# Kernel tuning notes

Hardware: AMD Instinct MI355X
Metric: run time of the kernel (lower is better)

Reference implementation:

```python
import jax, jax.numpy as jnp
import numpy as np
import math

N = 8192       # number of cells (spatial tokens)
D = 512        # d_model
H = 512        # attn_hidden_dim (defaults to d_model)
GAMMA = 0.5    # real/fake mixing weight


def setup_inputs() -> dict:
    key = jax.random.key(0)
    ks = jax.random.split(key, 9)
    s = 1.0 / math.sqrt(D)  # nn.Linear-like init scale -> stable exp(scores)
    x = jax.random.normal(ks[0], (N, D), dtype=jnp.float32)
    real_edge_mask = jax.random.bernoulli(ks[1], 0.5, (N, N))
    fake_edge_mask = jax.random.bernoulli(ks[2], 0.5, (N, N))
    Wq_real = jax.random.normal(ks[3], (D, H), dtype=jnp.float32) * s
    Wk_real = jax.random.normal(ks[4], (D, H), dtype=jnp.float32) * s
    Wq_fake = jax.random.normal(ks[5], (D, H), dtype=jnp.float32) * s
    Wk_fake = jax.random.normal(ks[6], (D, H), dtype=jnp.float32) * s
    Wv = jax.random.normal(ks[7], (D, D), dtype=jnp.float32) * s
    bv = jnp.zeros((D,), dtype=jnp.float32)
    return dict(x=x, real_edge_mask=real_edge_mask, fake_edge_mask=fake_edge_mask,
                Wq_real=Wq_real, Wk_real=Wk_real, Wq_fake=Wq_fake, Wk_fake=Wk_fake,
                Wv=Wv, bv=bv)


def reference(x, real_edge_mask, fake_edge_mask, Wq_real, Wk_real, Wq_fake, Wk_fake, Wv, bv):
    scale = 1.0 / math.sqrt(H)
    neg = jnp.float32(-1e9)
    # real branch scores [N, N]
    sr = jnp.einsum('nh,mh->nm', x @ Wq_real, x @ Wk_real) * scale
    sr = jnp.where(real_edge_mask, neg, sr)
    # fake branch scores [N, N]
    sf = jnp.einsum('nh,mh->nm', x @ Wq_fake, x @ Wk_fake) * scale
    sf = jnp.where(fake_edge_mask, neg, sf)
    # NOTE: original computes row maxima but never uses them (dead code);
    # it exponentiates raw scores directly -- replicated faithfully.
    scores = (jnp.exp(sr) + GAMMA * jnp.exp(sf)) / (1.0 + GAMMA)
    attn = scores / jnp.sum(scores, axis=-1, keepdims=True)
    V = x @ Wv + bv
    cntx = attn @ V
    return cntx, attn
```

## Files before the change

kernel.cpp:

```cpp
#include <hip/hip_runtime.h>


#define K_N 8192
#define K_D 512

typedef float  f32x4 __attribute__((ext_vector_type(4)));
typedef _Float16 f16x8 __attribute__((ext_vector_type(8)));
typedef unsigned short u16;
typedef unsigned int u32;

__device__ __forceinline__ u16 f2h(float f) {
  _Float16 h = (_Float16)f;
  return __builtin_bit_cast(u16, h);
}
__device__ __forceinline__ float h2f(u16 b) {
  return (float)__builtin_bit_cast(_Float16, b);
}

__device__ __forceinline__ void gload_lds16(const void* g, void* l) {
  __builtin_amdgcn_global_load_lds(
      (const __attribute__((address_space(1))) void*)g,
      (__attribute__((address_space(3))) void*)l, 16, 0, 0);
}

__device__ __forceinline__ void nt_store4(float* p, f32x4 v) {
  __builtin_nontemporal_store(v, (f32x4*)p);
}

__global__ void k_detect(const unsigned char* __restrict__ m, int* __restrict__ flag) {
  __shared__ int any;
  if (threadIdx.x == 0) any = 0;
  __syncthreads();
  int local = 0;
  for (int i = threadIdx.x; i < 65536; i += 256)
    local |= m[4 * i + 1];
  if (local) atomicOr(&any, 1);
  __syncthreads();
  if (threadIdx.x == 0) *flag = any ? 1 : 0;
}

__device__ __forceinline__ bool mask_at(const void* mask, int mode, size_t idx) {
  if (mode) return ((const unsigned char*)mask)[idx] != 0;
  return ((const int*)mask)[idx] != 0;
}

__device__ __forceinline__ u32 pack_word(const void* m, int mode, int r, int c) {
  u32 out = 0;
  if (mode) {
    const uint4* p = (const uint4*)((const unsigned char*)m + (size_t)r * K_N + c * 32);
    uint4 a = p[0], b = p[1];
    u32 ws[8] = {a.x, a.y, a.z, a.w, b.x, b.y, b.z, b.w};
#pragma unroll
    for (int i = 0; i < 8; i++) {
      u32 v = ws[i];
      v |= v >> 4; v |= v >> 2; v |= v >> 1;
      v &= 0x01010101u;
      out |= (v & 1u) << (4 * i);
      out |= ((v >> 8) & 1u) << (4 * i + 1);
      out |= ((v >> 16) & 1u) << (4 * i + 2);
      out |= ((v >> 24) & 1u) << (4 * i + 3);
    }
  } else {
    const uint4* p = (const uint4*)((const int*)m + (size_t)r * K_N + c * 32);
#pragma unroll
    for (int i = 0; i < 8; i++) {
      uint4 v = p[i];
      out |= (v.x ? 1u : 0u) << (4 * i);
      out |= (v.y ? 1u : 0u) << (4 * i + 1);
      out |= (v.z ? 1u : 0u) << (4 * i + 2);
      out |= (v.w ? 1u : 0u) << (4 * i + 3);
    }
  }
  return out;
}

__global__ __launch_bounds__(256) void k_packmask2(
    const void* __restrict__ mR, const void* __restrict__ mF,
    const int* __restrict__ flag,
    u32* __restrict__ bR, u32* __restrict__ bF,
    float* __restrict__ cntx) {
  __shared__ u32 sm[32][129];
  const int mode = *flag;
  const int tid = threadIdx.x;
  const int r0 = blockIdx.x * 128;
  const int c0 = blockIdx.y * 32;

  {
    float4* cz = (float4*)cntx;
    int bid = blockIdx.x + (blockIdx.y << 6);
#pragma unroll
    for (int i = 0; i < 8; ++i)
      cz[(size_t)bid * 2048 + i * 256 + tid] = make_float4(0.f, 0.f, 0.f, 0.f);
  }

#pragma unroll
  for (int t = 0; t < 2; ++t) {
    const void* m = t ? mF : mR;
    u32* dst = t ? bF : bR;
    if (t) __syncthreads();
#pragma unroll 4
    for (int i = 0; i < 16; ++i) {
      int idx = i * 256 + tid;
      int r = idx >> 5, c = idx & 31;
      sm[c][r] = pack_word(m, mode, r0 + r, c0 + c);
    }
    __syncthreads();
#pragma unroll 4
    for (int i = 0; i < 16; ++i) {
      int idx = i * 256 + tid;
      int c = idx >> 7, r = idx & 127;
      dst[(size_t)(c0 + c) * K_N + r0 + r] = sm[c][r];
    }
  }
}

__global__ void k_transpose_w(const float* __restrict__ w0, const float* __restrict__ w1,
                              const float* __restrict__ w2, const float* __restrict__ w3,
                              const float* __restrict__ w4, u16* __restrict__ out) {
  __shared__ u16 sm[64][65];
  const float* srcs[5] = {w0, w1, w2, w3, w4};
  const float* in = srcs[blockIdx.z];
  u16* dst = out + (size_t)blockIdx.z * 262144;
  int c0 = blockIdx.x * 64, r0 = blockIdx.y * 64;
#pragma unroll
  for (int e = 0; e < 16; e++) {
    int idx = e * 256 + threadIdx.x;
    int i = idx >> 6, j = idx & 63;
    sm[i][j] = f2h(in[(size_t)(r0 + i) * 512 + c0 + j]);
  }
  __syncthreads();
#pragma unroll
  for (int e = 0; e < 16; e++) {
    int idx = e * 256 + threadIdx.x;
    int j = idx >> 6, i = idx & 63;
    dst[(size_t)(c0 + j) * 512 + r0 + i] = sm[i][j];
  }
}

__global__ void k_transpose_v(const u16* __restrict__ in, u16* __restrict__ out,
                              int R, int C) {
  __shared__ u16 sm[64][65];
  int c0 = blockIdx.x * 64, r0 = blockIdx.y * 64;
#pragma unroll
  for (int e = 0; e < 16; e++) {
    int idx = e * 256 + threadIdx.x;
    int i = idx >> 6, j = idx & 63;
    sm[i][j] = in[(size_t)(r0 + i) * C + c0 + j];
  }
  __syncthreads();
#pragma unroll
  for (int e = 0; e < 16; e++) {
    int idx = e * 256 + threadIdx.x;
    int j = idx >> 6, i = idx & 63;
    out[(size_t)(c0 + j) * R + r0 + i] = sm[i][j];
  }
}

template <int A_F32>
__device__ __forceinline__ void gemm_core(const void* __restrict__ Ap, int lda,
                                          const u16* __restrict__ Bt, int ldb,
                                          int rowBase, int colBase, int K,
                                          u16* sA, u16* sB, f32x4 (&acc)[4][4]) {
  const int tid   = threadIdx.x;
  const int lane  = tid & 63;
  const int waveM = tid >> 7;
  const int waveN = (tid >> 6) & 1;
  const int lrow  = lane & 15;
  const int lk    = lane >> 4;

  for (int k0 = 0; k0 < K; k0 += 64) {
    __syncthreads();
#pragma unroll
    for (int g = 0; g < 4; g++) {
      int cid = g * 256 + tid;
      int row = cid >> 3;
      int pk  = cid & 7;
      int k16 = pk ^ (row & 7);
      if (A_F32) {
        const float* s = (const float*)Ap + (size_t)(rowBase + row) * lda + k0 + k16 * 8;
        float4 v0 = *(const float4*)s;
        float4 v1 = *(const float4*)(s + 4);
        ushort4 h0, h1;
        h0.x = f2h(v0.x); h0.y = f2h(v0.y); h0.z = f2h(v0.z); h0.w = f2h(v0.w);
        h1.x = f2h(v1.x); h1.y = f2h(v1.y); h1.z = f2h(v1.z); h1.w = f2h(v1.w);
        *(ushort4*)&sA[cid * 8]     = h0;
        *(ushort4*)&sA[cid * 8 + 4] = h1;
      } else {
        uint4 v = *(const uint4*)((const u16*)Ap + (size_t)(rowBase + row) * lda + k0 + k16 * 8);
        *(uint4*)&sA[cid * 8] = v;
      }
      uint4 w = *(const uint4*)(Bt + (size_t)(colBase + row) * ldb + k0 + k16 * 8);
      *(uint4*)&sB[cid * 8] = w;
    }
    __syncthreads();
#pragma unroll
    for (int kk = 0; kk < 2; kk++) {
      f16x8 af[4], bfv[4];
      int k16 = kk * 4 + lk;
#pragma unroll
      for (int mb = 0; mb < 4; mb++) {
        int r = waveM * 64 + mb * 16 + lrow;
        af[mb] = *(const f16x8*)&sA[r * 64 + ((k16 ^ (r & 7)) << 3)];
      }
#pragma unroll
      for (int nb = 0; nb < 4; nb++) {
        int c = waveN * 64 + nb * 16 + lrow;
        bfv[nb] = *(const f16x8*)&sB[c * 64 + ((k16 ^ (c & 7)) << 3)];
      }
#pragma unroll
      for (int mb = 0; mb < 4; mb++)
#pragma unroll
        for (int nb = 0; nb < 4; nb++)
          acc[mb][nb] = __builtin_amdgcn_mfma_f32_16x16x32_f16(af[mb], bfv[nb], acc[mb][nb], 0, 0, 0);
    }
  }
}

__global__ __launch_bounds__(256) void k_proj(const float* __restrict__ x,
                                              const u16* __restrict__ wt,
                                              u16* __restrict__ qr, u16* __restrict__ kr,
                                              u16* __restrict__ qf, u16* __restrict__ kf,
                                              u16* __restrict__ vh,
                                              const float* __restrict__ bv) {
  __shared__ u16 sA[128 * 64], sB[128 * 64];
  f32x4 acc[4][4] = {};
  const int z = blockIdx.z;
  const int rowBase = blockIdx.y * 128, colBase = blockIdx.x * 128;
  gemm_core<1>(x, K_D, wt + (size_t)z * 262144, K_D, rowBase, colBase, K_D, sA, sB, acc);

  u16* out = (z == 0) ? qr : (z == 1) ? kr : (z == 2) ? qf : (z == 3) ? kf : vh;
  const int lane = threadIdx.x & 63;
  const int waveM = threadIdx.x >> 7, waveN = (threadIdx.x >> 6) & 1;
  const int lrow = lane & 15, lk = lane >> 4;
#pragma unroll
  for (int mb = 0; mb < 4; mb++)
#pragma unroll
    for (int nb = 0; nb < 4; nb++)
#pragma unroll
      for (int r = 0; r < 4; r++) {
        int grow = rowBase + waveM * 64 + mb * 16 + lk * 4 + r;
        int gcol = colBase + waveN * 64 + nb * 16 + lrow;
        float v = acc[mb][nb][r];
        if (z == 4) v += bv[gcol];
        out[(size_t)grow * K_D + gcol] = f2h(v);
      }
}

__global__ __launch_bounds__(256, 2) void k_scores2(
    const u16* __restrict__ qr, const u16* __restrict__ kr,
    const u16* __restrict__ qf, const u16* __restrict__ kf,
    const u32* __restrict__ bitR, const u32* __restrict__ bitF,
    u16* __restrict__ outp, float* __restrict__ partial) {

  __shared__ u16 s[2][2][8192];

  const int tid = threadIdx.x;
  const int lane = tid & 63, wid = tid >> 6;

  int b = blockIdx.x + (blockIdx.y << 6);
  int xcd = b & 7, j = b >> 3;
  const int by = xcd * 8 + (j & 7);
  const int bx = j >> 3;
  const int rowBase = by * 128, colBase = bx * 128;

  const u16* qrB = qr + (size_t)rowBase * K_D;
  const u16* krB = kr + (size_t)colBase * K_D;
  const u16* qfB = qf + (size_t)rowBase * K_D;
  const u16* kfB = kf + (size_t)colBase * K_D;

  f32x4 accR[4][4] = {}, accF[4][4] = {};

  auto STAGE = [&](int buf, const u16* qb, const u16* kb, int k0) {
#pragma unroll
    for (int jj = 0; jj < 4; ++jj) {
      int cid = jj * 256 + tid;
      int row = cid >> 3;
      int k16 = (cid & 7) ^ (row & 7);
      gload_lds16(qb + (size_t)row * K_D + k0 + k16 * 8,
                  &s[buf][0][(jj * 256 + wid * 64) * 8]);
      gload_lds16(kb + (size_t)row * K_D + k0 + k16 * 8,
                  &s[buf][1][(jj * 256 + wid * 64) * 8]);
    }
  };

  const int waveM = wid >> 1;
  const int waveN = wid & 1;
  const int lrow = lane & 15, lk = lane >> 4;

  auto COMPUTE = [&](f32x4 (&acc)[4][4], int cur) {
#pragma unroll
    for (int kk = 0; kk < 2; ++kk) {
      int k16 = kk * 4 + lk;
      f16x8 a[4], bb[4];
#pragma unroll
      for (int mb = 0; mb < 4; ++mb) {
        int r = waveM * 64 + mb * 16 + lrow;
        a[mb] = *(const f16x8*)&s[cur][0][r * 64 + ((k16 ^ (r & 7)) << 3)];
      }
#pragma unroll
      for (int nb = 0; nb < 4; ++nb) {
        int c = waveN * 64 + nb * 16 + lrow;
        bb[nb] = *(const f16x8*)&s[cur][1][c * 64 + ((k16 ^ (c & 7)) << 3)];
      }
#pragma unroll
      for (int mb = 0; mb < 4; ++mb)
#pragma unroll
        for (int nb = 0; nb < 4; ++nb)
          acc[mb][nb] = __builtin_amdgcn_mfma_f32_16x16x32_f16(a[mb], bb[nb], acc[mb][nb], 0, 0, 0);
    }
  };

  STAGE(0, qrB, krB, 0);
  __syncthreads();
  int cur = 0;
  for (int it = 0; it < 8; ++it) {
    if (it < 7) STAGE(cur ^ 1, qrB, krB, (it + 1) * 64);
    else        STAGE(cur ^ 1, qfB, kfB, 0);
    COMPUTE(accR, cur);
    __syncthreads();
    cur ^= 1;
  }
  for (int it = 0; it < 8; ++it) {
    if (it < 7) STAGE(cur ^ 1, qfB, kfB, (it + 1) * 64);
    COMPUTE(accF, cur);
    __syncthreads();
    cur ^= 1;
  }

  const float scale = 0.04419417382415922f;
  u16* vt16 = (u16*)&s[0][0][0];

#pragma unroll
  for (int mb = 0; mb < 4; ++mb)
#pragma unroll
    for (int rr = 0; rr < 4; ++rr) {
      int growl = waveM * 64 + mb * 16 + lk * 4 + rr;
      int grow = rowBase + growl;
      u32 wR0 = bitR[(size_t)(bx * 4 + waveN * 2 + 0) * K_N + grow];
      u32 wR1 = bitR[(size_t)(bx * 4 + waveN * 2 + 1) * K_N + grow];
      u32 wF0 = bitF[(size_t)(bx * 4 + waveN * 2 + 0) * K_N + grow];
      u32 wF1 = bitF[(size_t)(bx * 4 + waveN * 2 + 1) * K_N + grow];
      float rs = 0.f;
#pragma unroll
      for (int nb = 0; nb < 4; ++nb) {
        int cc = nb * 16 + lrow;
        int gcoll = waveN * 64 + cc;
        u32 wR = (cc >> 5) ? wR1 : wR0;
        u32 wF = (cc >> 5) ? wF1 : wF0;
        int bitpos = cc & 31;
        bool m1 = (wR >> bitpos) & 1u;
        bool m2 = (wF >> bitpos) & 1u;
        float er = m1 ? 0.f : __expf(accR[mb][nb][rr] * scale);
        float ef = m2 ? 0.f : __expf(accF[mb][nb][rr] * scale);
        float v = er + 0.5f * ef;
        rs += v;
        vt16[growl * 136 + gcoll] = f2h(v);
      }
      rs += __shfl_xor(rs, 1, 64);
      rs += __shfl_xor(rs, 2, 64);
      rs += __shfl_xor(rs, 4, 64);
      rs += __shfl_xor(rs, 8, 64);
      if (lrow == 0)
        partial[(size_t)grow * 128 + bx * 2 + waveN] = rs;
    }
  __syncthreads();

#pragma unroll
  for (int jj = 0; jj < 8; ++jj) {
    int f = jj * 256 + tid;
    int row = f >> 4, seg = f & 15;
    uint4 v = *(const uint4*)&vt16[row * 136 + seg * 8];
    *(uint4*)&outp[(size_t)(rowBase + row) * K_N + colBase + seg * 8] = v;
  }
}

template <int F16OUT, int USEBITS>
__global__ __launch_bounds__(512, 2) void k_scores8(
    const u16* __restrict__ qr, const u16* __restrict__ kr,
    const u16* __restrict__ qf, const u16* __restrict__ kf,
    const u32* __restrict__ bitR, const u32* __restrict__ bitF,
    const void* __restrict__ mR, const void* __restrict__ mF,
    const int* __restrict__ flag,
    void* __restrict__ outp, float* __restrict__ partial) {

  __shared__ u16 s[2][4][8192];

  const int tid = threadIdx.x;
  const int lane = tid & 63, wid = tid >> 6;
  const int bx = blockIdx.x, by = blockIdx.y;
  const int rowBase = by * 128, colBase = bx * 128;

  const u16* base0 = qr + (size_t)rowBase * K_D;
  const u16* base1 = kr + (size_t)colBase * K_D;
  const u16* base2 = qf + (size_t)rowBase * K_D;
  const u16* base3 = kf + (size_t)colBase * K_D;

  f32x4 accR[4][2] = {}, accF[4][2] = {};

  auto STAGE = [&](int b, int k0) {
    const u16* bases[4] = {base0, base1, base2, base3};
#pragma unroll
    for (int t = 0; t < 4; ++t)
#pragma unroll
      for (int j = 0; j < 2; ++j) {
        int cid = j * 512 + tid;
        int row = cid >> 3;
        int k16 = (cid & 7) ^ (row & 7);
        gload_lds16(bases[t] + (size_t)row * K_D + k0 + k16 * 8,
                    &s[b][t][(j * 512 + wid * 64) * 8]);
      }
  };

  STAGE(0, 0);
  __syncthreads();

  const int waveM = wid >> 2, waveN = wid & 3;
  const int lrow = lane & 15, lk = lane >> 4;

  int cur = 0;
  for (int it = 0; it < 8; ++it) {
    if (it < 7) STAGE(cur ^ 1, (it + 1) * 64);
#pragma unroll
    for (int kk = 0; kk < 2; ++kk) {
      int k16 = kk * 4 + lk;
      f16x8 aR[4], aF[4], bR[2], bF[2];
#pragma unroll
      for (int mb = 0; mb < 4; ++mb) {
        int r = waveM * 64 + mb * 16 + lrow;
        int off = r * 64 + ((k16 ^ (r & 7)) << 3);
        aR[mb] = *(const f16x8*)&s[cur][0][off];
        aF[mb] = *(const f16x8*)&s[cur][2][off];
      }
#pragma unroll
      for (int nb = 0; nb < 2; ++nb) {
        int c = waveN * 32 + nb * 16 + lrow;
        int off = c * 64 + ((k16 ^ (c & 7)) << 3);
        bR[nb] = *(const f16x8*)&s[cur][1][off];
        bF[nb] = *(const f16x8*)&s[cur][3][off];
      }
#pragma unroll
      for (int mb = 0; mb < 4; ++mb)
#pragma unroll
        for (int nb = 0; nb < 2; ++nb) {
          accR[mb][nb] = __builtin_amdgcn_mfma_f32_16x16x32_f16(aR[mb], bR[nb], accR[mb][nb], 0, 0, 0);
          accF[mb][nb] = __builtin_amdgcn_mfma_f32_16x16x32_f16(aF[mb], bF[nb], accF[mb][nb], 0, 0, 0);
        }
    }
    __syncthreads();
    cur ^= 1;
  }

  const float scale = 0.04419417382415922f;
  const int mode = USEBITS ? 0 : *flag;
  u16*   vt16 = (u16*)&s[0][0][0];
  float* vt32 = (float*)&s[0][0][0];

#pragma unroll
  for (int mb = 0; mb < 4; ++mb)
#pragma unroll
    for (int rr = 0; rr < 4; ++rr) {
      int growl = waveM * 64 + mb * 16 + lk * 4 + rr;
      int grow = rowBase + growl;
      u32 wR = 0, wF = 0;
      if (USEBITS) {
        wR = bitR[(size_t)(bx * 4 + waveN) * K_N + grow];
        wF = bitF[(size_t)(bx * 4 + waveN) * K_N + grow];
      }
      float rs = 0.f;
#pragma unroll
      for (int nb = 0; nb < 2; ++nb) {
        int bitpos = nb * 16 + lrow;
        int gcoll = waveN * 32 + bitpos;
        bool m1, m2;
        if (USEBITS) {
          m1 = (wR >> bitpos) & 1u;
          m2 = (wF >> bitpos) & 1u;
        } else {
          size_t oi = (size_t)grow * K_N + colBase + gcoll;
          m1 = mask_at(mR, mode, oi);
          m2 = mask_at(mF, mode, oi);
        }
        float er = m1 ? 0.f : __expf(accR[mb][nb][rr] * scale);
        float ef = m2 ? 0.f : __expf(accF[mb][nb][rr] * scale);
        float v = er + 0.5f * ef;
        rs += v;
        if (F16OUT) vt16[growl * 136 + gcoll] = f2h(v);
        else        vt32[growl * 132 + gcoll] = v;
      }
      rs += __shfl_xor(rs, 1, 64);
      rs += __shfl_xor(rs, 2, 64);
      rs += __shfl_xor(rs, 4, 64);
      rs += __shfl_xor(rs, 8, 64);
      if (lrow == 0)
        partial[(size_t)grow * 256 + bx * 4 + waveN] = rs;
    }
  __syncthreads();

  if (F16OUT) {
    u16* out = (u16*)outp;
#pragma unroll
    for (int j = 0; j < 4; ++j) {
      int f = j * 512 + tid;
      int row = f >> 4, seg = f & 15;
      uint4 v = *(const uint4*)&vt16[row * 136 + seg * 8];
      *(uint4*)&out[(size_t)(rowBase + row) * K_N + colBase + seg * 8] = v;
    }
  } else {
    float* out = (float*)outp;
#pragma unroll
    for (int j = 0; j < 8; ++j) {
      int f = j * 512 + tid;
      int row = f >> 5, seg = f & 31;
      float4 v = *(const float4*)&vt32[row * 132 + seg * 4];
      *(float4*)&out[(size_t)(rowBase + row) * K_N + colBase + seg * 4] = v;
    }
  }
}

template <int STRIDE>
__global__ void k_rowsum(const float* __restrict__ partial, float* __restrict__ inv) {
  int r = blockIdx.x * 256 + threadIdx.x;
  const float4* p = (const float4*)(partial + (size_t)r * STRIDE);
  float s = 0.f;
#pragma unroll 8
  for (int j = 0; j < STRIDE / 4; j++) {
    float4 v = p[j];
    s += v.x + v.y + v.z + v.w;
  }
  inv[r] = 1.0f / s;
}

__global__ void k_norm_b(float* __restrict__ attn, const float* __restrict__ inv) {
  const size_t total = (size_t)K_N * K_N / 4;
  for (size_t i = (size_t)blockIdx.x * 256 + threadIdx.x; i < total;
       i += (size_t)gridDim.x * 256) {
    int row = (int)(i >> 11);
    float s = inv[row];
    float4 v = ((float4*)attn)[i];
    v.x *= s; v.y *= s; v.z *= s; v.w *= s;
    ((float4*)attn)[i] = v;
  }
}

__global__ __launch_bounds__(256, 4) void k_cntx6(
    const u16* __restrict__ sh, const u16* __restrict__ vT,
    const float* __restrict__ inv, float* __restrict__ cntx,
    float* __restrict__ attn) {
  __shared__ u16 sA[128 * 64], sB[128 * 64];
  f32x4 acc[4][4] = {};

  const int tid = threadIdx.x;
  int b = blockIdx.x + (blockIdx.y << 3);
  int xcd = b & 7, j = b >> 3;
  const int s  = xcd + 8 * (j >> 4);
  const int u  = j & 15;
  const int ch = u >> 2;
  const int ks = u & 3;
  const int rowBase = s * 128, colBase = ch * 128;
  const int k0 = ks * 2048;

  gemm_core<0>(sh + (size_t)k0, K_N, vT + (size_t)k0, K_N,
               rowBase, colBase, 2048, sA, sB, acc);

  const int lane = tid & 63;
  const int waveM = tid >> 7, waveN = (tid >> 6) & 1;
  const int lrow = lane & 15, lk = lane >> 4;
#pragma unroll
  for (int mb = 0; mb < 4; mb++)
#pragma unroll
    for (int rr = 0; rr < 4; rr++) {
      int grow = rowBase + waveM * 64 + mb * 16 + lk * 4 + rr;
      float iv = inv[grow];
#pragma unroll
      for (int nb = 0; nb < 4; nb++) {
        int gcol = colBase + waveN * 64 + nb * 16 + lrow;
        atomicAdd(&cntx[(size_t)grow * K_D + gcol], acc[mb][nb][rr] * iv);
      }
    }

  const int ac0 = ks * 2048 + ch * 512;
  const u16* src = sh + (size_t)rowBase * K_N + ac0;
  float* ad = attn + (size_t)rowBase * K_N + ac0;
  for (int i = tid; i < 128 * 64; i += 256) {
    int row = i >> 6, c8 = i & 63;
    float sc = inv[rowBase + row];
    uint4 v = *(const uint4*)&src[(size_t)row * K_N + c8 * 8];
    f32x4 o0, o1;
    o0.x = h2f(v.x & 0xFFFF) * sc; o0.y = h2f(v.x >> 16) * sc;
    o0.z = h2f(v.y & 0xFFFF) * sc; o0.w = h2f(v.y >> 16) * sc;
    o1.x = h2f(v.z & 0xFFFF) * sc; o1.y = h2f(v.z >> 16) * sc;
    o1.z = h2f(v.w & 0xFFFF) * sc; o1.w = h2f(v.w >> 16) * sc;
    float* d2 = ad + (size_t)row * K_N + c8 * 8;
    nt_store4(d2, o0);
    nt_store4(d2 + 4, o1);
  }
}

template <int A_F32>
__global__ __launch_bounds__(256) void k_cntx(const void* __restrict__ Ap,
                                              const u16* __restrict__ vT,
                                              const float* __restrict__ inv,
                                              float* __restrict__ out) {
  __shared__ u16 sA[128 * 64], sB[128 * 64];
  f32x4 acc[4][4] = {};
  int b = blockIdx.x + blockIdx.y * 4;
  int c = b & 7, jj = b >> 3;
  int xb = jj & 3, yb = c + 8 * (jj >> 2);
  const int rowBase = yb * 128, colBase = xb * 128;
  gemm_core<A_F32>(Ap, K_N, vT, K_N, rowBase, colBase, K_N, sA, sB, acc);

  const int lane = threadIdx.x & 63;
  const int waveM = threadIdx.x >> 7, waveN = (threadIdx.x >> 6) & 1;
  const int lrow = lane & 15, lk = lane >> 4;
#pragma unroll
  for (int mb = 0; mb < 4; mb++)
#pragma unroll
    for (int r = 0; r < 4; r++) {
      int grow = rowBase + waveM * 64 + mb * 16 + lk * 4 + r;
      float iv = inv[grow];
#pragma unroll
      for (int nb = 0; nb < 4; nb++) {
        int gcol = colBase + waveN * 64 + nb * 16 + lrow;
        out[(size_t)grow * K_D + gcol] = acc[mb][nb][r] * iv;
      }
    }
}

extern "C" void kernel_launch(void* const* d_in, const int* in_sizes, int n_in,
                              void* d_out, int out_size, void* d_ws, size_t ws_size,
                              hipStream_t stream) {
  const float* x   = (const float*)d_in[0];
  const void*  mR  = d_in[1];
  const void*  mF  = d_in[2];
  const float* Wv  = (const float*)d_in[7];
  const float* bv  = (const float*)d_in[8];

  const size_t ND = (size_t)K_N * K_D;
  u16* xh = (u16*)d_ws;
  u16* qr = xh + ND;
  u16* kr = qr + ND;
  u16* qf = kr + ND;
  u16* kf = qf + ND;
  u16* vh = kf + ND;
  u16* vT = vh + ND;
  u16* wt = vT + ND;
  u32* bitR = (u32*)(wt + 5 * 262144);
  u32* bitF = bitR + (size_t)K_N * 256;
  u16* sh   = (u16*)(bitF + (size_t)K_N * 256);

  const size_t need_bits = (size_t)((char*)sh - (char*)d_ws) + 64;
  const size_t need_sh   = (size_t)((char*)sh - (char*)d_ws) + (size_t)K_N * K_N * 2;
  const bool have_bits = ws_size >= need_bits;
  const bool have_sh   = ws_size >= need_sh;

  float* cntx = (float*)d_out;
  float* attn = cntx + ND;
  float* partial = (float*)d_ws;
  float* inv     = (float*)qr;
  int* flag = have_bits ? (int*)sh : (int*)cntx;

  k_detect<<<1, 256, 0, stream>>>((const unsigned char*)mR, flag);
  if (have_bits)
    k_packmask2<<<dim3(64, 8), 256, 0, stream>>>(mR, mF, flag, bitR, bitF, cntx);

  k_transpose_w<<<dim3(8, 8, 5), 256, 0, stream>>>(
      (const float*)d_in[3], (const float*)d_in[4], (const float*)d_in[5],
      (const float*)d_in[6], Wv, wt);

  k_proj<<<dim3(4, 64, 5), 256, 0, stream>>>(x, wt, qr, kr, qf, kf, vh, bv);
  k_transpose_v<<<dim3(8, 128), 256, 0, stream>>>(vh, vT, K_N, K_D);

  if (have_sh && have_bits) {
    k_scores2<<<dim3(64, 64), 256, 0, stream>>>(qr, kr, qf, kf, bitR, bitF, sh, partial);
    k_rowsum<128><<<32, 256, 0, stream>>>(partial, inv);
    k_cntx6<<<dim3(8, 128), 256, 0, stream>>>(sh, vT, inv, cntx, attn);
  } else if (have_bits) {
    k_scores8<0, 1><<<dim3(64, 64), 512, 0, stream>>>(qr, kr, qf, kf, bitR, bitF,
                                                      mR, mF, flag, attn, partial);
    k_rowsum<256><<<32, 256, 0, stream>>>(partial, inv);
    k_cntx<1><<<dim3(4, 64), 256, 0, stream>>>(attn, vT, inv, cntx);
    k_norm_b<<<8192, 256, 0, stream>>>(attn, inv);
  } else {
    k_scores8<0, 0><<<dim3(64, 64), 512, 0, stream>>>(qr, kr, qf, kf, nullptr, nullptr,
                                                      mR, mF, flag, attn, partial);
    k_rowsum<256><<<32, 256, 0, stream>>>(partial, inv);
    k_cntx<1><<<dim3(4, 64), 256, 0, stream>>>(attn, vT, inv, cntx);
    k_norm_b<<<8192, 256, 0, stream>>>(attn, inv);
  }
}
```

Measured before the change: 574.8 us.

## Single-buffer scores kernel with one accumulator set to raise occupancy to three blocks

Rewrites the dual-branch score kernel so the real and fake branches run one after another with a single accumulator set instead of two. The real-branch exp values are written to the output, then read back and combined with the fake branch. LDS drops from double-buffered to single-buffered and launch bounds are raised to allow three blocks per CU. This trades away the load/compute overlap of double buffering and adds an extra global write and read of the tile in exchange for lower register and LDS pressure and higher occupancy.

```diff
diff --git a/kernel.cpp b/kernel.cpp
--- a/kernel.cpp
+++ b/kernel.cpp
@@ -246,13 +246,15 @@
       }
 }
 
-__global__ __launch_bounds__(256, 2) void k_scores2(
+__global__ __launch_bounds__(256, 3) void k_scores3(
     const u16* __restrict__ qr, const u16* __restrict__ kr,
     const u16* __restrict__ qf, const u16* __restrict__ kf,
     const u32* __restrict__ bitR, const u32* __restrict__ bitF,
     u16* __restrict__ outp, float* __restrict__ partial) {
 
-  __shared__ u16 s[2][2][8192];
+  __shared__ u16 smem[17408];
+  u16* sQ = smem;
+  u16* sK = smem + 8192;
 
   const int tid = threadIdx.x;
   const int lane = tid & 63, wid = tid >> 6;
@@ -268,26 +270,28 @@
   const u16* qfB = qf + (size_t)rowBase * K_D;
   const u16* kfB = kf + (size_t)colBase * K_D;
 
-  f32x4 accR[4][4] = {}, accF[4][4] = {};
-
-  auto STAGE = [&](int buf, const u16* qb, const u16* kb, int k0) {
+  const int waveM = wid >> 1;
+  const int waveN = wid & 1;
+  const int lrow = lane & 15, lk = lane >> 4;
+  const float scale = 0.04419417382415922f;
+  u16* vt16 = smem;
+
+  f32x4 acc[4][4];
+
+  auto STAGE = [&](const u16* qb, const u16* kb, int k0) {
 #pragma unroll
     for (int jj = 0; jj < 4; ++jj) {
       int cid = jj * 256 + tid;
       int row = cid >> 3;
       int k16 = (cid & 7) ^ (row & 7);
       gload_lds16(qb + (size_t)row * K_D + k0 + k16 * 8,
-                  &s[buf][0][(jj * 256 + wid * 64) * 8]);
+                  &sQ[(jj * 256 + wid * 64) * 8]);
       gload_lds16(kb + (size_t)row * K_D + k0 + k16 * 8,
-                  &s[buf][1][(jj * 256 + wid * 64) * 8]);
+                  &sK[(jj * 256 + wid * 64) * 8]);
     }
   };
 
-  const int waveM = wid >> 1;
-  const int waveN = wid & 1;
-  const int lrow = lane & 15, lk = lane >> 4;
-
-  auto COMPUTE = [&](f32x4 (&acc)[4][4], int cur) {
+  auto COMPUTE = [&]() {
 #pragma unroll
     for (int kk = 0; kk < 2; ++kk) {
       int k16 = kk * 4 + lk;
@@ -295,12 +299,12 @@
 #pragma unroll
       for (int mb = 0; mb < 4; ++mb) {
         int r = waveM * 64 + mb * 16 + lrow;
-        a[mb] = *(const f16x8*)&s[cur][0][r * 64 + ((k16 ^ (r & 7)) << 3)];
+        a[mb] = *(const f16x8*)&sQ[r * 64 + ((k16 ^ (r & 7)) << 3)];
       }
 #pragma unroll
       for (int nb = 0; nb < 4; ++nb) {
         int c = waveN * 64 + nb * 16 + lrow;
-        bb[nb] = *(const f16x8*)&s[cur][1][c * 64 + ((k16 ^ (c & 7)) << 3)];
+        bb[nb] = *(const f16x8*)&sK[c * 64 + ((k16 ^ (c & 7)) << 3)];
       }
 #pragma unroll
       for (int mb = 0; mb < 4; ++mb)
@@ -310,25 +314,19 @@
     }
   };
 
-  STAGE(0, qrB, krB, 0);
-  __syncthreads();
-  int cur = 0;
-  for (int it = 0; it < 8; ++it) {
-    if (it < 7) STAGE(cur ^ 1, qrB, krB, (it + 1) * 64);
-    else        STAGE(cur ^ 1, qfB, kfB, 0);
-    COMPUTE(accR, cur);
+#pragma unroll
+  for (int mb = 0; mb < 4; ++mb)
+#pragma unroll
+    for (int nb = 0; nb < 4; ++nb)
+      acc[mb][nb] = (f32x4){0.f, 0.f, 0.f, 0.f};
+
+  for (int t = 0; t < 8; ++t) {
     __syncthreads();
-    cur ^= 1;
-  }
-  for (int it = 0; it < 8; ++it) {
-    if (it < 7) STAGE(cur ^ 1, qfB, kfB, (it + 1) * 64);
-    COMPUTE(accF, cur);
+    STAGE(qrB, krB, t * 64);
     __syncthreads();
-    cur ^= 1;
-  }
-
-  const float scale = 0.04419417382415922f;
-  u16* vt16 = (u16*)&s[0][0][0];
+    COMPUTE();
+  }
+  __syncthreads();
 
 #pragma unroll
   for (int mb = 0; mb < 4; ++mb)
@@ -338,21 +336,65 @@
       int grow = rowBase + growl;
       u32 wR0 = bitR[(size_t)(bx * 4 + waveN * 2 + 0) * K_N + grow];
       u32 wR1 = bitR[(size_t)(bx * 4 + waveN * 2 + 1) * K_N + grow];
-      u32 wF0 = bitF[(size_t)(bx * 4 + waveN * 2 + 0) * K_N + grow];
-      u32 wF1 = bitF[(size_t)(bx * 4 + waveN * 2 + 1) * K_N + grow];
-      float rs = 0.f;
 #pragma unroll
       for (int nb = 0; nb < 4; ++nb) {
         int cc = nb * 16 + lrow;
         int gcoll = waveN * 64 + cc;
         u32 wR = (cc >> 5) ? wR1 : wR0;
+        bool m1 = (wR >> (cc & 31)) & 1u;
+        float er = m1 ? 0.f : __expf(acc[mb][nb][rr] * scale);
+        vt16[growl * 136 + gcoll] = f2h(er);
+      }
+    }
+  __syncthreads();
+#pragma unroll
+  for (int jj = 0; jj < 8; ++jj) {
+    int f = jj * 256 + tid;
+    int row = f >> 4, seg = f & 15;
+    uint4 v = *(const uint4*)&vt16[row * 136 + seg * 8];
+    *(uint4*)&outp[(size_t)(rowBase + row) * K_N + colBase + seg * 8] = v;
+  }
+
+#pragma unroll
+  for (int mb = 0; mb < 4; ++mb)
+#pragma unroll
+    for (int nb = 0; nb < 4; ++nb)
+      acc[mb][nb] = (f32x4){0.f, 0.f, 0.f, 0.f};
+
+  for (int t = 0; t < 8; ++t) {
+    __syncthreads();
+    STAGE(qfB, kfB, t * 64);
+    __syncthreads();
+    COMPUTE();
+  }
+  __syncthreads();
+
+#pragma unroll
+  for (int jj = 0; jj < 8; ++jj) {
+    int f = jj * 256 + tid;
+    int row = f >> 4, seg = f & 15;
+    uint4 v = *(const uint4*)&outp[(size_t)(rowBase + row) * K_N + colBase + seg * 8];
+    *(uint4*)&vt16[row * 136 + seg * 8] = v;
+  }
+  __syncthreads();
+
+#pragma unroll
+  for (int mb = 0; mb < 4; ++mb)
+#pragma unroll
+    for (int rr = 0; rr < 4; ++rr) {
+      int growl = waveM * 64 + mb * 16 + lk * 4 + rr;
+      int grow = rowBase + growl;
+      u32 wF0 = bitF[(size_t)(bx * 4 + waveN * 2 + 0) * K_N + grow];
+      u32 wF1 = bitF[(size_t)(bx * 4 + waveN * 2 + 1) * K_N + grow];
+      float rs = 0.f;
+#pragma unroll
+      for (int nb = 0; nb < 4; ++nb) {
+        int cc = nb * 16 + lrow;
+        int gcoll = waveN * 64 + cc;
         u32 wF = (cc >> 5) ? wF1 : wF0;
-        int bitpos = cc & 31;
-        bool m1 = (wR >> bitpos) & 1u;
-        bool m2 = (wF >> bitpos) & 1u;
-        float er = m1 ? 0.f : __expf(accR[mb][nb][rr] * scale);
-        float ef = m2 ? 0.f : __expf(accF[mb][nb][rr] * scale);
-        float v = er + 0.5f * ef;
+        bool m2 = (wF >> (cc & 31)) & 1u;
+        float ef = m2 ? 0.f : __expf(acc[mb][nb][rr] * scale);
+        float v = h2f(vt16[growl * 136 + gcoll]) + 0.5f * ef;
         rs += v;
         vt16[growl * 136 + gcoll] = f2h(v);
       }
@@ -364,7 +406,6 @@
         partial[(size_t)grow * 128 + bx * 2 + waveN] = rs;
     }
   __syncthreads();
-
 #pragma unroll
   for (int jj = 0; jj < 8; ++jj) {
     int f = jj * 256 + tid;
@@ -671,7 +712,7 @@
   k_transpose_v<<<dim3(8, 128), 256, 0, stream>>>(vh, vT, K_N, K_D);
 
   if (have_sh && have_bits) {
-    k_scores2<<<dim3(64, 64), 256, 0, stream>>>(qr, kr, qf, kf, bitR, bitF, sh, partial);
+    k_scores3<<<dim3(64, 64), 256, 0, stream>>>(qr, kr, qf, kf, bitR, bitF, sh, partial);
     k_rowsum<128><<<32, 256, 0, stream>>>(partial, inv);
     k_cntx6<<<dim3(8, 128), 256, 0, stream>>>(sh, vT, inv, cntx, attn);
   } else if (have_bits) {
```

Result: slower. 605.9 us (+5.4%).
